# Performance work log

Hardware: AMD Instinct MI355X
Metric: run time of the kernel (lower is better)

The kernel has to match this reference:

```python
import jax, jax.numpy as jnp
import numpy as np

DIM = 256
HEADS = 4
B, N = 2, 4096
NEG = -1e9
EPS = 1e-5


def setup_inputs() -> dict:
    key = jax.random.key(0)
    ks = jax.random.split(key, 12)
    s = 0.02
    inp = {
        "x": jax.random.normal(ks[0], (B, N, DIM), dtype=jnp.float32),
        "adj": jax.random.randint(ks[1], (B, N, N), 0, 2, dtype=jnp.int32),
        "Wq": jax.random.normal(ks[2], (DIM, DIM), dtype=jnp.float32) * s,
        "bq": jnp.zeros((DIM,), jnp.float32),
        "Wk": jax.random.normal(ks[3], (DIM, DIM), dtype=jnp.float32) * s,
        "bk": jnp.zeros((DIM,), jnp.float32),
        "Wv": jax.random.normal(ks[4], (DIM, DIM), dtype=jnp.float32) * s,
        "bv": jnp.zeros((DIM,), jnp.float32),
        "Wo": jax.random.normal(ks[5], (DIM, DIM), dtype=jnp.float32) * s,
        "bo": jnp.zeros((DIM,), jnp.float32),
        "gamma": jnp.ones((DIM,), jnp.float32),
        "beta": jnp.zeros((DIM,), jnp.float32),
    }
    return inp


def reference(x, adj, Wq, bq, Wk, bk, Wv, bv, Wo, bo, gamma, beta):
    Bx, Nx, C = x.shape
    H = HEADS
    D = C // H
    scale = D ** (-0.5)
    # torch Linear: y = x @ W.T + b
    def proj(W, b):
        return (x @ W.T + b).reshape(Bx, Nx, H, D).transpose(0, 2, 1, 3)  # [B,H,N,D]
    q = proj(Wq, bq)
    k = proj(Wk, bk)
    v = proj(Wv, bv)
    attn = jnp.einsum("bhnd,bhmd->bhnm", q, k) * scale          # [B,H,N,N]
    attn = jnp.where(adj[:, None, :, :] == 0, NEG, attn)
    attn = jax.nn.softmax(attn, axis=-1)
    # dropout omitted (eval mode / deterministic reference)
    out = jnp.einsum("bhnm,bhmd->bhnd", attn, v)                # [B,H,N,D]
    out = out.transpose(0, 2, 1, 3).reshape(Bx, Nx, C)
    out = out @ Wo.T + bo
    mu = jnp.mean(out, axis=-1, keepdims=True)
    var = jnp.var(out, axis=-1, keepdims=True)
    return (out - mu) * jax.lax.rsqrt(var + EPS) * gamma + beta
```

## Files before the change

### kernel.cpp

```cpp
#include <hip/hip_runtime.h>
#include <stdint.h>

#define CDIM 256
#define HEADS 4
#define HD 64
#define NB 2
#define NN 4096

typedef unsigned short u16;
typedef unsigned long long u64;
typedef __attribute__((ext_vector_type(8))) short short8;
typedef __attribute__((ext_vector_type(4))) float f32x4;

#define QSCALE 0.1803368801111244f

__device__ __forceinline__ u16 f2bf(float f) {
  union { float f; unsigned u; } v; v.f = f;
  return (u16)((v.u + 0x7fffu + ((v.u >> 16) & 1u)) >> 16);
}
__device__ __forceinline__ float bf2f(u16 u) {
  union { unsigned u; float f; } v; v.u = ((unsigned)u) << 16; return v.f;
}

__global__ __launch_bounds__(256) void prep(
    const int* __restrict__ adj, u64* __restrict__ bm,
    const float* __restrict__ Wq, const float* __restrict__ Wk,
    const float* __restrict__ Wv, const float* __restrict__ Wo,
    u16* __restrict__ Wqb, u16* __restrict__ Wkb,
    u16* __restrict__ Wvb, u16* __restrict__ Wob) {
  if (blockIdx.x < 16384) {
    const int wave = threadIdx.x >> 6, lane = threadIdx.x & 63;
    const size_t widx = (size_t)blockIdx.x * 4 + wave;
    const size_t base = widx * 512;
#pragma unroll
    for (int it = 0; it < 8; ++it) {
      int a = adj[base + it * 64 + lane];
      u64 m = __ballot(a != 0);
      if (lane == 0) bm[widx * 8 + it] = m;
    }
  } else {
    int bi = blockIdx.x - 16384;
    size_t base = ((size_t)bi * 256 + threadIdx.x) * 8;
    int w = (int)(base >> 16);
    size_t lo = base & 65535;
    const float* src;
    u16* dst;
    if (w == 0)      { src = Wq + lo; dst = Wqb + lo; }
    else if (w == 1) { src = Wk + lo; dst = Wkb + lo; }
    else if (w == 2) { src = Wv + lo; dst = Wvb + lo; }
    else             { src = Wo + lo; dst = Wob + lo; }
    float4 a = reinterpret_cast<const float4*>(src)[0];
    float4 b = reinterpret_cast<const float4*>(src)[1];
    short8 h;
    h[0] = (short)f2bf(a.x); h[1] = (short)f2bf(a.y);
    h[2] = (short)f2bf(a.z); h[3] = (short)f2bf(a.w);
    h[4] = (short)f2bf(b.x); h[5] = (short)f2bf(b.y);
    h[6] = (short)f2bf(b.z); h[7] = (short)f2bf(b.w);
    *reinterpret_cast<short8*>(dst) = h;
  }
}

__device__ __forceinline__ short8 fragf32(const float* p) {
  float4 a = reinterpret_cast<const float4*>(p)[0];
  float4 b = reinterpret_cast<const float4*>(p)[1];
  short8 h;
  h[0] = (short)f2bf(a.x); h[1] = (short)f2bf(a.y);
  h[2] = (short)f2bf(a.z); h[3] = (short)f2bf(a.w);
  h[4] = (short)f2bf(b.x); h[5] = (short)f2bf(b.y);
  h[6] = (short)f2bf(b.z); h[7] = (short)f2bf(b.w);
  return h;
}

__global__ __launch_bounds__(256) void qkv_gemm(
    const float* __restrict__ x,
    const u16* __restrict__ Wqb, const u16* __restrict__ Wkb,
    const u16* __restrict__ Wvb,
    const float* __restrict__ bq, const float* __restrict__ bk,
    const float* __restrict__ bv,
    u16* __restrict__ Qb, u16* __restrict__ Kb, u16* __restrict__ Vtb) {
  const int tid = threadIdx.x, w = tid >> 6, lane = tid & 63;
  const int quad = lane >> 4, l15 = lane & 15;
  const int tok0 = blockIdx.x * 16;
  const int b = tok0 >> 12, nl = tok0 & 4095;
  const int ym = blockIdx.y;

  f32x4 acc[4];
#pragma unroll
  for (int i = 0; i < 4; ++i) acc[i] = (f32x4){0.f, 0.f, 0.f, 0.f};

  if (ym < 2) {
    const u16* Wb = (ym == 0) ? Wqb : Wkb;
    const float* bias = (ym == 0) ? bq : bk;
    const float scale = (ym == 0) ? QSCALE : 1.0f;
    u16* outp = (ym == 0) ? Qb : Kb;
#pragma unroll
    for (int ks = 0; ks < 8; ++ks) {
      short8 af = fragf32(x + (size_t)(tok0 + l15) * 256 + ks * 32 + quad * 8);
#pragma unroll
      for (int ns = 0; ns < 4; ++ns) {
        short8 bf = *reinterpret_cast<const short8*>(
            &Wb[(size_t)(w * 64 + ns * 16 + l15) * 256 + ks * 32 + quad * 8]);
        acc[ns] = __builtin_amdgcn_mfma_f32_16x16x32_bf16(af, bf, acc[ns], 0, 0, 0);
      }
    }
#pragma unroll
    for (int ns = 0; ns < 4; ++ns) {
      int d = ns * 16 + l15;
      float bb = bias[w * 64 + d];
#pragma unroll
      for (int r = 0; r < 4; ++r) {
        int tok = nl + quad * 4 + r;
        outp[((size_t)(b * HEADS + w) * NN + tok) * HD + d] =
            f2bf((acc[ns][r] + bb) * scale);
      }
    }
  } else {
#pragma unroll
    for (int ks = 0; ks < 8; ++ks) {
      short8 xf = fragf32(x + (size_t)(tok0 + l15) * 256 + ks * 32 + quad * 8);
#pragma unroll
      for (int ms = 0; ms < 4; ++ms) {
        short8 wf = *reinterpret_cast<const short8*>(
            &Wvb[(size_t)(w * 64 + ms * 16 + l15) * 256 + ks * 32 + quad * 8]);
        acc[ms] = __builtin_amdgcn_mfma_f32_16x16x32_bf16(wf, xf, acc[ms], 0, 0, 0);
      }
    }
#pragma unroll
    for (int ms = 0; ms < 4; ++ms) {
#pragma unroll
      for (int r = 0; r < 4; ++r) {
        int d = ms * 16 + quad * 4 + r;
        float bb = bv[w * 64 + d];
        Vtb[((size_t)((b * HEADS + w) * HD + d)) * NN + nl + l15] =
            f2bf(acc[ms][r] + bb);
      }
    }
  }
}

__global__ __launch_bounds__(256) void attn_mfma(
    const u16* __restrict__ Qb, const u16* __restrict__ Kb,
    const u16* __restrict__ Vtb, const u64* __restrict__ bm,
    u16* __restrict__ Opb, float* __restrict__ Lp) {
  __shared__ u16 Ks[64 * 72];
  __shared__ u16 Vs[64 * 72];
  __shared__ u16 Ps[4][16 * 72];

  const int tid = threadIdx.x;
  const int wave = tid >> 6, lane = tid & 63;
  const int quad = lane >> 4, l15 = lane & 15;
  const int bh = blockIdx.y, b = bh >> 2, h = bh & 3;
  const int q0 = blockIdx.x * 64 + wave * 16;
  const int half = blockIdx.z;
  const int key0 = half * 2048;

  const u16* qr = Qb + ((size_t)bh * NN + q0 + l15) * HD + quad * 8;
  const short8 qf0 = *reinterpret_cast<const short8*>(qr);
  const short8 qf1 = *reinterpret_cast<const short8*>(qr + 32);

  f32x4 Oacc[4];
#pragma unroll
  for (int i = 0; i < 4; ++i) Oacc[i] = (f32x4){0.f, 0.f, 0.f, 0.f};
  float li[4] = {0.f, 0.f, 0.f, 0.f};
  const f32x4 z4 = {0.f, 0.f, 0.f, 0.f};
  u16* Pw = &Ps[wave][0];
  const u64* bmr = bm + ((size_t)b * NN + q0 + quad * 4) * 64 + half * 32;

  const u16* kbase = Kb + (size_t)bh * NN * HD;
  const u16* vbase = Vtb + (size_t)bh * HD * NN;
  const int rr = tid >> 3, cc8 = (tid & 7) * 8;
  const int rr2 = rr + 32;

  uint4 k0, k1, v0, v1;
  k0 = *reinterpret_cast<const uint4*>(kbase + (size_t)(key0 + rr) * HD + cc8);
  k1 = *reinterpret_cast<const uint4*>(kbase + (size_t)(key0 + rr2) * HD + cc8);
  v0 = *reinterpret_cast<const uint4*>(vbase + (size_t)rr * NN + key0 + cc8);
  v1 = *reinterpret_cast<const uint4*>(vbase + (size_t)rr2 * NN + key0 + cc8);

  for (int mt = 0; mt < 32; ++mt) {
    __syncthreads();
    *reinterpret_cast<uint4*>(&Ks[rr * 72 + cc8]) = k0;
    *reinterpret_cast<uint4*>(&Ks[rr2 * 72 + cc8]) = k1;
    *reinterpret_cast<uint4*>(&Vs[rr * 72 + cc8]) = v0;
    *reinterpret_cast<uint4*>(&Vs[rr2 * 72 + cc8]) = v1;
    __syncthreads();
    if (mt + 1 < 32) {
      int kb2 = key0 + (mt + 1) * 64;
      k0 = *reinterpret_cast<const uint4*>(kbase + (size_t)(kb2 + rr) * HD + cc8);
      k1 = *reinterpret_cast<const uint4*>(kbase + (size_t)(kb2 + rr2) * HD + cc8);
      v0 = *reinterpret_cast<const uint4*>(vbase + (size_t)rr * NN + kb2 + cc8);
      v1 = *reinterpret_cast<const uint4*>(vbase + (size_t)rr2 * NN + kb2 + cc8);
    }

    u64 am[4];
#pragma unroll
    for (int r = 0; r < 4; ++r) am[r] = bmr[r * 64 + mt];

#pragma unroll
    for (int t = 0; t < 4; ++t) {
      const u16* kr = &Ks[(t * 16 + l15) * 72 + quad * 8];
      short8 kf0 = *reinterpret_cast<const short8*>(kr);
      short8 kf1 = *reinterpret_cast<const short8*>(kr + 32);
      f32x4 s = __builtin_amdgcn_mfma_f32_16x16x32_bf16(qf0, kf0, z4, 0, 0, 0);
      s = __builtin_amdgcn_mfma_f32_16x16x32_bf16(qf1, kf1, s, 0, 0, 0);
      const int sh = t * 16 + l15;
#pragma unroll
      for (int r = 0; r < 4; ++r) {
        float p = ((unsigned)(am[r] >> sh) & 1u) ? exp2f(s[r]) : 0.f;
        li[r] += p;
        Pw[(quad * 4 + r) * 72 + sh] = (u16)(__float_as_uint(p) >> 16);
      }
    }
    __asm__ volatile("s_waitcnt lgkmcnt(0)" ::: "memory");

    const short8 pf0 = *reinterpret_cast<const short8*>(&Pw[l15 * 72 + quad * 8]);
    const short8 pf1 = *reinterpret_cast<const short8*>(&Pw[l15 * 72 + 32 + quad * 8]);
#pragma unroll
    for (int dt = 0; dt < 4; ++dt) {
      const u16* vr = &Vs[(dt * 16 + l15) * 72 + quad * 8];
      short8 vf0 = *reinterpret_cast<const short8*>(vr);
      short8 vf1 = *reinterpret_cast<const short8*>(vr + 32);
      Oacc[dt] = __builtin_amdgcn_mfma_f32_16x16x32_bf16(pf0, vf0, Oacc[dt], 0, 0, 0);
      Oacc[dt] = __builtin_amdgcn_mfma_f32_16x16x32_bf16(pf1, vf1, Oacc[dt], 0, 0, 0);
    }
  }

  u16* ob = Opb + (size_t)(half * NB + b) * NN * CDIM;
#pragma unroll
  for (int r = 0; r < 4; ++r) {
    float lt = li[r];
#pragma unroll
    for (int off = 1; off < 16; off <<= 1) lt += __shfl_xor(lt, off, 64);
    int tok = q0 + quad * 4 + r;
    if (l15 == 0) Lp[((size_t)half * 8 + bh) * NN + tok] = lt;
#pragma unroll
    for (int dt = 0; dt < 4; ++dt)
      ob[(size_t)tok * CDIM + h * HD + dt * 16 + l15] = f2bf(Oacc[dt][r]);
  }
}

__global__ __launch_bounds__(256) void comb_oproj(
    const u16* __restrict__ Opb, const float* __restrict__ Lp,
    const u16* __restrict__ Wob, const float* __restrict__ bo,
    const float* __restrict__ gamma, const float* __restrict__ beta,
    float* __restrict__ out) {
  __shared__ u16 As[16 * 264];
  __shared__ float ys[16][264];
  __shared__ float linv[64];
  const int tid = threadIdx.x, w = tid >> 6, lane = tid & 63;
  const int quad = lane >> 4, l15 = lane & 15;
  const int tok0 = blockIdx.x * 16;
  const int b = tok0 >> 12, nl = tok0 & 4095;

  if (tid < 64) {
    int tokr = tid >> 2, hh = tid & 3;
    int bh = b * 4 + hh;
    int n = nl + tokr;
    float s = Lp[(size_t)bh * NN + n] + Lp[(size_t)(8 + bh) * NN + n];
    linv[tokr * 4 + hh] = (s > 0.f) ? (1.f / s) : 0.f;
  }
  __syncthreads();

  {
    int tokr = tid >> 4, ch0 = (tid & 15) * 16;
    size_t base = ((size_t)b * NN + nl + tokr) * CDIM + ch0;
    uint4 a0 = *reinterpret_cast<const uint4*>(Opb + base);
    uint4 a1 = *reinterpret_cast<const uint4*>(Opb + base + 8);
    uint4 c0 = *reinterpret_cast<const uint4*>(Opb + 2097152 + base);
    uint4 c1 = *reinterpret_cast<const uint4*>(Opb + 2097152 + base + 8);
    float inv = linv[tokr * 4 + (ch0 >> 6)];
    unsigned wa[8] = {a0.x, a0.y, a0.z, a0.w, a1.x, a1.y, a1.z, a1.w};
    unsigned wb[8] = {c0.x, c0.y, c0.z, c0.w, c1.x, c1.y, c1.z, c1.w};
    u16 ov[16];
#pragma unroll
    for (int i = 0; i < 8; ++i) {
      float lo = (bf2f((u16)(wa[i] & 0xffffu)) + bf2f((u16)(wb[i] & 0xffffu))) * inv;
      float hi = (bf2f((u16)(wa[i] >> 16)) + bf2f((u16)(wb[i] >> 16))) * inv;
      ov[2 * i] = f2bf(lo);
      ov[2 * i + 1] = f2bf(hi);
    }
    u16* dst = &As[tokr * 264 + ch0];
    *reinterpret_cast<uint4*>(dst) = *reinterpret_cast<uint4*>(ov);
    *reinterpret_cast<uint4*>(dst + 8) = *reinterpret_cast<uint4*>(ov + 8);
  }
  __syncthreads();

  f32x4 acc[4];
#pragma unroll
  for (int i = 0; i < 4; ++i) acc[i] = (f32x4){0.f, 0.f, 0.f, 0.f};
#pragma unroll
  for (int ks = 0; ks < 8; ++ks) {
    short8 af = *reinterpret_cast<const short8*>(&As[l15 * 264 + ks * 32 + quad * 8]);
#pragma unroll
    for (int ns = 0; ns < 4; ++ns) {
      short8 bf = *reinterpret_cast<const short8*>(
          &Wob[(size_t)(w * 64 + ns * 16 + l15) * 256 + ks * 32 + quad * 8]);
      acc[ns] = __builtin_amdgcn_mfma_f32_16x16x32_bf16(af, bf, acc[ns], 0, 0, 0);
    }
  }

#pragma unroll
  for (int ns = 0; ns < 4; ++ns) {
    int ch = w * 64 + ns * 16 + l15;
    float bb = bo[ch];
#pragma unroll
    for (int r = 0; r < 4; ++r) ys[quad * 4 + r][ch] = acc[ns][r] + bb;
  }
  __syncthreads();

  float g[4], bt[4];
#pragma unroll
  for (int i = 0; i < 4; ++i) {
    g[i] = gamma[lane + i * 64];
    bt[i] = beta[lane + i * 64];
  }
#pragma unroll
  for (int rr = 0; rr < 4; ++rr) {
    int r = w * 4 + rr;
    float v[4], s = 0.f, s2 = 0.f;
#pragma unroll
    for (int i = 0; i < 4; ++i) {
      v[i] = ys[r][lane + i * 64];
      s += v[i];
      s2 = fmaf(v[i], v[i], s2);
    }
#pragma unroll
    for (int off = 32; off > 0; off >>= 1) {
      s += __shfl_xor(s, off, 64);
      s2 += __shfl_xor(s2, off, 64);
    }
    float mu = s * (1.f / 256.f);
    float rs = rsqrtf(s2 * (1.f / 256.f) - mu * mu + 1e-5f);
    float* orow = out + (size_t)(tok0 + r) * 256;
#pragma unroll
    for (int i = 0; i < 4; ++i)
      orow[lane + i * 64] = (v[i] - mu) * rs * g[i] + bt[i];
  }
}

extern "C" void kernel_launch(void* const* d_in, const int* in_sizes, int n_in,
                              void* d_out, int out_size, void* d_ws, size_t ws_size,
                              hipStream_t stream) {
  const float* x     = (const float*)d_in[0];
  const int*   adj   = (const int*)d_in[1];
  const float* Wq    = (const float*)d_in[2];
  const float* bq    = (const float*)d_in[3];
  const float* Wk    = (const float*)d_in[4];
  const float* bk    = (const float*)d_in[5];
  const float* Wv    = (const float*)d_in[6];
  const float* bv    = (const float*)d_in[7];
  const float* Wo    = (const float*)d_in[8];
  const float* bo    = (const float*)d_in[9];
  const float* gamma = (const float*)d_in[10];
  const float* beta  = (const float*)d_in[11];
  float* out = (float*)d_out;

  const size_t PER = (size_t)NB * HEADS * NN * HD;
  u16* Wqb = (u16*)d_ws;
  u16* Wkb = Wqb + 65536;
  u16* Wvb = Wkb + 65536;
  u16* Wob = Wvb + 65536;
  u64* bmp = (u64*)(Wob + 65536);
  u16* Qb  = (u16*)(bmp + 524288);
  u16* Kb  = Qb + PER;
  u16* Vtb = Kb + PER;
  u16* Opb = Vtb + PER;
  float* Lp = (float*)(Opb + 2 * PER);

  const size_t NEED = (size_t)((u16*)(Lp + 65536) - (u16*)d_ws) * sizeof(u16);
  if (ws_size < NEED) return;

  prep<<<dim3(16512), dim3(256), 0, stream>>>(
      adj, bmp, Wq, Wk, Wv, Wo, Wqb, Wkb, Wvb, Wob);

  qkv_gemm<<<dim3(512, 3), dim3(256), 0, stream>>>(
      x, Wqb, Wkb, Wvb, bq, bk, bv, Qb, Kb, Vtb);

  attn_mfma<<<dim3(NN / 64, NB * HEADS, 2), dim3(256), 0, stream>>>(
      Qb, Kb, Vtb, bmp, Opb, Lp);

  comb_oproj<<<dim3((NB * NN) / 16), dim3(256), 0, stream>>>(
      Opb, Lp, Wob, bo, gamma, beta, out);
}
```

Before: 353.1 us.

## Fuse all stages into one persistent cooperative kernel with grid syncs

```diff
diff --git a/kernel.cpp b/kernel.cpp
--- a/kernel.cpp
+++ b/kernel.cpp
@@ -1,5 +1,8 @@
 #include <hip/hip_runtime.h>
+#include <hip/hip_cooperative_groups.h>
 #include <stdint.h>
+
+namespace cg = cooperative_groups;
 
 #define CDIM 256
 #define HEADS 4
@@ -21,45 +24,6 @@
 __device__ __forceinline__ float bf2f(u16 u) {
   union { unsigned u; float f; } v; v.u = ((unsigned)u) << 16; return v.f;
 }
-
-__global__ __launch_bounds__(256) void prep(
-    const int* __restrict__ adj, u64* __restrict__ bm,
-    const float* __restrict__ Wq, const float* __restrict__ Wk,
-    const float* __restrict__ Wv, const float* __restrict__ Wo,
-    u16* __restrict__ Wqb, u16* __restrict__ Wkb,
-    u16* __restrict__ Wvb, u16* __restrict__ Wob) {
-  if (blockIdx.x < 16384) {
-    const int wave = threadIdx.x >> 6, lane = threadIdx.x & 63;
-    const size_t widx = (size_t)blockIdx.x * 4 + wave;
-    const size_t base = widx * 512;
-#pragma unroll
-    for (int it = 0; it < 8; ++it) {
-      int a = adj[base + it * 64 + lane];
-      u64 m = __ballot(a != 0);
-      if (lane == 0) bm[widx * 8 + it] = m;
-    }
-  } else {
-    int bi = blockIdx.x - 16384;
-    size_t base = ((size_t)bi * 256 + threadIdx.x) * 8;
-    int w = (int)(base >> 16);
-    size_t lo = base & 65535;
-    const float* src;
-    u16* dst;
-    if (w == 0)      { src = Wq + lo; dst = Wqb + lo; }
-    else if (w == 1) { src = Wk + lo; dst = Wkb + lo; }
-    else if (w == 2) { src = Wv + lo; dst = Wvb + lo; }
-    else             { src = Wo + lo; dst = Wob + lo; }
-    float4 a = reinterpret_cast<const float4*>(src)[0];
-    float4 b = reinterpret_cast<const float4*>(src)[1];
-    short8 h;
-    h[0] = (short)f2bf(a.x); h[1] = (short)f2bf(a.y);
-    h[2] = (short)f2bf(a.z); h[3] = (short)f2bf(a.w);
-    h[4] = (short)f2bf(b.x); h[5] = (short)f2bf(b.y);
-    h[6] = (short)f2bf(b.z); h[7] = (short)f2bf(b.w);
-    *reinterpret_cast<short8*>(dst) = h;
-  }
-}
-
 __device__ __forceinline__ short8 fragf32(const float* p) {
   float4 a = reinterpret_cast<const float4*>(p)[0];
   float4 b = reinterpret_cast<const float4*>(p)[1];
@@ -71,8 +35,38 @@
   return h;
 }
 
-__global__ __launch_bounds__(256) void qkv_gemm(
-    const float* __restrict__ x,
+__device__ __forceinline__ void adj_unit(int u, const int* __restrict__ adj,
+                                         u64* __restrict__ bm) {
+  const int wave = threadIdx.x >> 6, lane = threadIdx.x & 63;
+  const size_t widx = (size_t)u * 4 + wave;
+  const size_t base = widx * 512;
+#pragma unroll
+  for (int it = 0; it < 8; ++it) {
+    int a = adj[base + it * 64 + lane];
+    u64 m = __ballot(a != 0);
+    if (lane == 0) bm[widx * 8 + it] = m;
+  }
+}
+
+__device__ __forceinline__ void wconv_unit(
+    int bi, const float* __restrict__ Wq, const float* __restrict__ Wk,
+    const float* __restrict__ Wv, const float* __restrict__ Wo,
+    u16* __restrict__ Wqb, u16* __restrict__ Wkb,
+    u16* __restrict__ Wvb, u16* __restrict__ Wob) {
+  size_t base = ((size_t)bi * 256 + threadIdx.x) * 8;
+  int w = (int)(base >> 16);
+  size_t lo = base & 65535;
+  const float* src;
+  u16* dst;
+  if (w == 0)      { src = Wq + lo; dst = Wqb + lo; }
+  else if (w == 1) { src = Wk + lo; dst = Wkb + lo; }
+  else if (w == 2) { src = Wv + lo; dst = Wvb + lo; }
+  else             { src = Wo + lo; dst = Wob + lo; }
+  *reinterpret_cast<short8*>(dst) = fragf32(src);
+}
+
+__device__ __forceinline__ void qkv_unit(
+    int ym, int bx, const float* __restrict__ x,
     const u16* __restrict__ Wqb, const u16* __restrict__ Wkb,
     const u16* __restrict__ Wvb,
     const float* __restrict__ bq, const float* __restrict__ bk,
@@ -80,9 +74,8 @@
     u16* __restrict__ Qb, u16* __restrict__ Kb, u16* __restrict__ Vtb) {
   const int tid = threadIdx.x, w = tid >> 6, lane = tid & 63;
   const int quad = lane >> 4, l15 = lane & 15;
-  const int tok0 = blockIdx.x * 16;
+  const int tok0 = bx * 16;
   const int b = tok0 >> 12, nl = tok0 & 4095;
-  const int ym = blockIdx.y;
 
   f32x4 acc[4];
 #pragma unroll
@@ -138,20 +131,20 @@
   }
 }
 
-__global__ __launch_bounds__(256) void attn_mfma(
+__device__ __forceinline__ void attn_unit(
+    int bx, int bh, int half, char* smem,
     const u16* __restrict__ Qb, const u16* __restrict__ Kb,
     const u16* __restrict__ Vtb, const u64* __restrict__ bm,
     u16* __restrict__ Opb, float* __restrict__ Lp) {
-  __shared__ u16 Ks[64 * 72];
-  __shared__ u16 Vs[64 * 72];
-  __shared__ u16 Ps[4][16 * 72];
+  u16* Ks = (u16*)smem;
+  u16* Vs = Ks + 64 * 72;
+  u16* Ps = Vs + 64 * 72;
 
   const int tid = threadIdx.x;
   const int wave = tid >> 6, lane = tid & 63;
   const int quad = lane >> 4, l15 = lane & 15;
-  const int bh = blockIdx.y, b = bh >> 2, h = bh & 3;
-  const int q0 = blockIdx.x * 64 + wave * 16;
-  const int half = blockIdx.z;
+  const int b = bh >> 2, h = bh & 3;
+  const int q0 = bx * 64 + wave * 16;
   const int key0 = half * 2048;
 
   const u16* qr = Qb + ((size_t)bh * NN + q0 + l15) * HD + quad * 8;
@@ -163,7 +156,7 @@
   for (int i = 0; i < 4; ++i) Oacc[i] = (f32x4){0.f, 0.f, 0.f, 0.f};
   float li[4] = {0.f, 0.f, 0.f, 0.f};
   const f32x4 z4 = {0.f, 0.f, 0.f, 0.f};
-  u16* Pw = &Ps[wave][0];
+  u16* Pw = Ps + wave * 16 * 72;
   const u64* bmr = bm + ((size_t)b * NN + q0 + quad * 4) * 64 + half * 32;
 
   const u16* kbase = Kb + (size_t)bh * NN * HD;
@@ -225,7 +218,7 @@
     }
   }
 
-  u16* ob = Opb + (size_t)(half * NB + b) * NN * CDIM;
+  u16* ob = Opb + (size_t)(half * NB + (bh >> 2)) * NN * CDIM;
 #pragma unroll
   for (int r = 0; r < 4; ++r) {
     float lt = li[r];
@@ -239,17 +232,17 @@
   }
 }
 
-__global__ __launch_bounds__(256) void comb_oproj(
-    const u16* __restrict__ Opb, const float* __restrict__ Lp,
-    const u16* __restrict__ Wob, const float* __restrict__ bo,
-    const float* __restrict__ gamma, const float* __restrict__ beta,
-    float* __restrict__ out) {
-  __shared__ u16 As[16 * 264];
-  __shared__ float ys[16][264];
-  __shared__ float linv[64];
+__device__ __forceinline__ void comb_unit(
+    int bx, char* smem, const u16* __restrict__ Opb,
+    const float* __restrict__ Lp, const u16* __restrict__ Wob,
+    const float* __restrict__ bo, const float* __restrict__ gamma,
+    const float* __restrict__ beta, float* __restrict__ out) {
+  u16* As = (u16*)smem;
+  float* ys = (float*)(smem + 8448);
+  float* linv = (float*)(smem + 8448 + 16896);
   const int tid = threadIdx.x, w = tid >> 6, lane = tid & 63;
   const int quad = lane >> 4, l15 = lane & 15;
-  const int tok0 = blockIdx.x * 16;
+  const int tok0 = bx * 16;
   const int b = tok0 >> 12, nl = tok0 & 4095;
 
   if (tid < 64) {
@@ -304,7 +297,7 @@
     int ch = w * 64 + ns * 16 + l15;
     float bb = bo[ch];
 #pragma unroll
-    for (int r = 0; r < 4; ++r) ys[quad * 4 + r][ch] = acc[ns][r] + bb;
+    for (int r = 0; r < 4; ++r) ys[(quad * 4 + r) * 264 + ch] = acc[ns][r] + bb;
   }
   __syncthreads();
 
@@ -320,7 +313,7 @@
     float v[4], s = 0.f, s2 = 0.f;
 #pragma unroll
     for (int i = 0; i < 4; ++i) {
-      v[i] = ys[r][lane + i * 64];
+      v[i] = ys[r * 264 + lane + i * 64];
       s += v[i];
       s2 = fmaf(v[i], v[i], s2);
     }
@@ -336,6 +329,62 @@
     for (int i = 0; i < 4; ++i)
       orow[lane + i * 64] = (v[i] - mu) * rs * g[i] + bt[i];
   }
+}
+
+__global__ __launch_bounds__(256, 4) void fused(
+    const float* x, const int* adj,
+    const float* Wq, const float* bq, const float* Wk, const float* bk,
+    const float* Wv, const float* bv, const float* Wo, const float* bo,
+    const float* gamma, const float* beta, float* out,
+    u16* Wqb, u16* Wkb, u16* Wvb, u16* Wob, u64* bmp,
+    u16* Qb, u16* Kb, u16* Vtb, u16* Opb, float* Lp) {
+  __shared__ __align__(16) char smem[27648];
+  const int blk = blockIdx.x;
+  cg::grid_group grid = cg::this_grid();
+
+  if (blk < 128) wconv_unit(blk, Wq, Wk, Wv, Wo, Wqb, Wkb, Wvb, Wob);
+#pragma unroll 1
+  for (int i = 0; i < 8; ++i) adj_unit(blk * 8 + i, adj, bmp);
+  grid.sync();
+
+#pragma unroll 1
+  for (int u = blk; u < 1536; u += 1024)
+    qkv_unit(u >> 9, u & 511, x, Wqb, Wkb, Wvb, bq, bk, bv, Qb, Kb, Vtb);
+#pragma unroll 1
+  for (int i = 0; i < 8; ++i) adj_unit(8192 + blk * 8 + i, adj, bmp);
+  grid.sync();
+
+  attn_unit(blk & 63, (blk >> 6) & 7, blk >> 9, smem,
+            Qb, Kb, Vtb, bmp, Opb, Lp);
+  grid.sync();
+
+  if (blk < 512)
+    comb_unit(blk, smem, Opb, Lp, Wob, bo, gamma, beta, out);
+}
+
+__global__ __launch_bounds__(256) void prep_k(
+    const int* adj, u64* bmp, const float* Wq, const float* Wk,
+    const float* Wv, const float* Wo, u16* Wqb, u16* Wkb, u16* Wvb, u16* Wob) {
+  if (blockIdx.x < 16384) adj_unit(blockIdx.x, adj, bmp);
+  else wconv_unit(blockIdx.x - 16384, Wq, Wk, Wv, Wo, Wqb, Wkb, Wvb, Wob);
+}
+__global__ __launch_bounds__(256) void qkv_k(
+    const float* x, const u16* Wqb, const u16* Wkb, const u16* Wvb,
+    const float* bq, const float* bk, const float* bv,
+    u16* Qb, u16* Kb, u16* Vtb) {
+  qkv_unit(blockIdx.y, blockIdx.x, x, Wqb, Wkb, Wvb, bq, bk, bv, Qb, Kb, Vtb);
+}
+__global__ __launch_bounds__(256) void attn_k(
+    const u16* Qb, const u16* Kb, const u16* Vtb, const u64* bmp,
+    u16* Opb, float* Lp) {
+  __shared__ __align__(16) char smem[27648];
+  attn_unit(blockIdx.x, blockIdx.y, blockIdx.z, smem, Qb, Kb, Vtb, bmp, Opb, Lp);
+}
+__global__ __launch_bounds__(256) void comb_k(
+    const u16* Opb, const float* Lp, const u16* Wob, const float* bo,
+    const float* gamma, const float* beta, float* out) {
+  __shared__ __align__(16) char smem[25600];
+  comb_unit(blockIdx.x, smem, Opb, Lp, Wob, bo, gamma, beta, out);
 }
 
 extern "C" void kernel_launch(void* const* d_in, const int* in_sizes, int n_in,
@@ -370,15 +419,24 @@
   const size_t NEED = (size_t)((u16*)(Lp + 65536) - (u16*)d_ws) * sizeof(u16);
   if (ws_size < NEED) return;
 
-  prep<<<dim3(16512), dim3(256), 0, stream>>>(
-      adj, bmp, Wq, Wk, Wv, Wo, Wqb, Wkb, Wvb, Wob);
-
-  qkv_gemm<<<dim3(512, 3), dim3(256), 0, stream>>>(
-      x, Wqb, Wkb, Wvb, bq, bk, bv, Qb, Kb, Vtb);
-
-  attn_mfma<<<dim3(NN / 64, NB * HEADS, 2), dim3(256), 0, stream>>>(
-      Qb, Kb, Vtb, bmp, Opb, Lp);
-
-  comb_oproj<<<dim3((NB * NN) / 16), dim3(256), 0, stream>>>(
-      Opb, Lp, Wob, bo, gamma, beta, out);
-}
+  void* args[] = {
+      (void*)&x, (void*)&adj, (void*)&Wq, (void*)&bq, (void*)&Wk, (void*)&bk,
+      (void*)&Wv, (void*)&bv, (void*)&Wo, (void*)&bo, (void*)&gamma,
+      (void*)&beta, (void*)&out, (void*)&Wqb, (void*)&Wkb, (void*)&Wvb,
+      (void*)&Wob, (void*)&bmp, (void*)&Qb, (void*)&Kb, (void*)&Vtb,
+      (void*)&Opb, (void*)&Lp};
+  hipError_t rc = hipLaunchCooperativeKernel(
+      (void*)fused, dim3(1024), dim3(256), args, 0, stream);
+
+  if (rc != hipSuccess) {
+    (void)hipGetLastError();
+    prep_k<<<dim3(16512), dim3(256), 0, stream>>>(
+        adj, bmp, Wq, Wk, Wv, Wo, Wqb, Wkb, Wvb, Wob);
+    qkv_k<<<dim3(512, 3), dim3(256), 0, stream>>>(
+        x, Wqb, Wkb, Wvb, bq, bk, bv, Qb, Kb, Vtb);
+    attn_k<<<dim3(64, 8, 2), dim3(256), 0, stream>>>(
+        Qb, Kb, Vtb, bmp, Opb, Lp);
+    comb_k<<<dim3(512), dim3(256), 0, stream>>>(
+        Opb, Lp, Wob, bo, gamma, beta, out);
+  }
+}
```

Result: slower. 764.6 us (+116.5%).

## Merge prep and QKV GEMM into one launch; compute row sums via MFMA

Applied to the files above, without the earlier changes.

```diff
diff --git a/kernel.cpp b/kernel.cpp
--- a/kernel.cpp
+++ b/kernel.cpp
@@ -21,45 +21,6 @@
 __device__ __forceinline__ float bf2f(u16 u) {
   union { unsigned u; float f; } v; v.u = ((unsigned)u) << 16; return v.f;
 }
-
-__global__ __launch_bounds__(256) void prep(
-    const int* __restrict__ adj, u64* __restrict__ bm,
-    const float* __restrict__ Wq, const float* __restrict__ Wk,
-    const float* __restrict__ Wv, const float* __restrict__ Wo,
-    u16* __restrict__ Wqb, u16* __restrict__ Wkb,
-    u16* __restrict__ Wvb, u16* __restrict__ Wob) {
-  if (blockIdx.x < 16384) {
-    const int wave = threadIdx.x >> 6, lane = threadIdx.x & 63;
-    const size_t widx = (size_t)blockIdx.x * 4 + wave;
-    const size_t base = widx * 512;
-#pragma unroll
-    for (int it = 0; it < 8; ++it) {
-      int a = adj[base + it * 64 + lane];
-      u64 m = __ballot(a != 0);
-      if (lane == 0) bm[widx * 8 + it] = m;
-    }
-  } else {
-    int bi = blockIdx.x - 16384;
-    size_t base = ((size_t)bi * 256 + threadIdx.x) * 8;
-    int w = (int)(base >> 16);
-    size_t lo = base & 65535;
-    const float* src;
-    u16* dst;
-    if (w == 0)      { src = Wq + lo; dst = Wqb + lo; }
-    else if (w == 1) { src = Wk + lo; dst = Wkb + lo; }
-    else if (w == 2) { src = Wv + lo; dst = Wvb + lo; }
-    else             { src = Wo + lo; dst = Wob + lo; }
-    float4 a = reinterpret_cast<const float4*>(src)[0];
-    float4 b = reinterpret_cast<const float4*>(src)[1];
-    short8 h;
-    h[0] = (short)f2bf(a.x); h[1] = (short)f2bf(a.y);
-    h[2] = (short)f2bf(a.z); h[3] = (short)f2bf(a.w);
-    h[4] = (short)f2bf(b.x); h[5] = (short)f2bf(b.y);
-    h[6] = (short)f2bf(b.z); h[7] = (short)f2bf(b.w);
-    *reinterpret_cast<short8*>(dst) = h;
-  }
-}
-
 __device__ __forceinline__ short8 fragf32(const float* p) {
   float4 a = reinterpret_cast<const float4*>(p)[0];
   float4 b = reinterpret_cast<const float4*>(p)[1];
@@ -71,25 +32,37 @@
   return h;
 }
 
-__global__ __launch_bounds__(256) void qkv_gemm(
-    const float* __restrict__ x,
-    const u16* __restrict__ Wqb, const u16* __restrict__ Wkb,
-    const u16* __restrict__ Wvb,
+__device__ __forceinline__ void adj_unit(int u, const int* __restrict__ adj,
+                                         u64* __restrict__ bm) {
+  const int wave = threadIdx.x >> 6, lane = threadIdx.x & 63;
+  const size_t widx = (size_t)u * 4 + wave;
+  const size_t base = widx * 512;
+#pragma unroll
+  for (int it = 0; it < 8; ++it) {
+    int a = adj[base + it * 64 + lane];
+    u64 m = __ballot(a != 0);
+    if (lane == 0) bm[widx * 8 + it] = m;
+  }
+}
+
+__device__ __forceinline__ void qkv_unit(
+    int ym, int bx, const float* __restrict__ x,
+    const float* __restrict__ Wq, const float* __restrict__ Wk,
+    const float* __restrict__ Wv,
     const float* __restrict__ bq, const float* __restrict__ bk,
     const float* __restrict__ bv,
     u16* __restrict__ Qb, u16* __restrict__ Kb, u16* __restrict__ Vtb) {
   const int tid = threadIdx.x, w = tid >> 6, lane = tid & 63;
   const int quad = lane >> 4, l15 = lane & 15;
-  const int tok0 = blockIdx.x * 16;
+  const int tok0 = bx * 16;
   const int b = tok0 >> 12, nl = tok0 & 4095;
-  const int ym = blockIdx.y;
 
   f32x4 acc[4];
 #pragma unroll
   for (int i = 0; i < 4; ++i) acc[i] = (f32x4){0.f, 0.f, 0.f, 0.f};
 
   if (ym < 2) {
-    const u16* Wb = (ym == 0) ? Wqb : Wkb;
+    const float* W = (ym == 0) ? Wq : Wk;
     const float* bias = (ym == 0) ? bq : bk;
     const float scale = (ym == 0) ? QSCALE : 1.0f;
     u16* outp = (ym == 0) ? Qb : Kb;
@@ -98,8 +71,8 @@
       short8 af = fragf32(x + (size_t)(tok0 + l15) * 256 + ks * 32 + quad * 8);
 #pragma unroll
       for (int ns = 0; ns < 4; ++ns) {
-        short8 bf = *reinterpret_cast<const short8*>(
-            &Wb[(size_t)(w * 64 + ns * 16 + l15) * 256 + ks * 32 + quad * 8]);
+        short8 bf = fragf32(
+            W + (size_t)(w * 64 + ns * 16 + l15) * 256 + ks * 32 + quad * 8);
         acc[ns] = __builtin_amdgcn_mfma_f32_16x16x32_bf16(af, bf, acc[ns], 0, 0, 0);
       }
     }
@@ -120,8 +93,8 @@
       short8 xf = fragf32(x + (size_t)(tok0 + l15) * 256 + ks * 32 + quad * 8);
 #pragma unroll
       for (int ms = 0; ms < 4; ++ms) {
-        short8 wf = *reinterpret_cast<const short8*>(
-            &Wvb[(size_t)(w * 64 + ms * 16 + l15) * 256 + ks * 32 + quad * 8]);
+        short8 wf = fragf32(
+            Wv + (size_t)(w * 64 + ms * 16 + l15) * 256 + ks * 32 + quad * 8);
         acc[ms] = __builtin_amdgcn_mfma_f32_16x16x32_bf16(wf, xf, acc[ms], 0, 0, 0);
       }
     }
@@ -135,6 +108,25 @@
             f2bf(acc[ms][r] + bb);
       }
     }
+  }
+}
+
+__global__ __launch_bounds__(256) void l1_prep_qkv(
+    const float* __restrict__ x, const int* __restrict__ adj,
+    const float* __restrict__ Wq, const float* __restrict__ Wk,
+    const float* __restrict__ Wv, const float* __restrict__ Wo,
+    const float* __restrict__ bq, const float* __restrict__ bk,
+    const float* __restrict__ bv,
+    u64* __restrict__ bmp, u16* __restrict__ Qb, u16* __restrict__ Kb,
+    u16* __restrict__ Vtb, u16* __restrict__ Wob) {
+  const int blk = blockIdx.x;
+  if (blk < 1536) {
+    qkv_unit(blk >> 9, blk & 511, x, Wq, Wk, Wv, bq, bk, bv, Qb, Kb, Vtb);
+  } else if (blk < 17920) {
+    adj_unit(blk - 1536, adj, bmp);
+  } else {
+    size_t base = ((size_t)(blk - 17920) * 256 + threadIdx.x) * 8;
+    *reinterpret_cast<short8*>(Wob + base) = fragf32(Wo + base);
   }
 }
 
@@ -158,10 +150,14 @@
   const short8 qf0 = *reinterpret_cast<const short8*>(qr);
   const short8 qf1 = *reinterpret_cast<const short8*>(qr + 32);
 
+  short8 ones;
+#pragma unroll
+  for (int i = 0; i < 8; ++i) ones[i] = (short)0x3F80;
+
   f32x4 Oacc[4];
 #pragma unroll
   for (int i = 0; i < 4; ++i) Oacc[i] = (f32x4){0.f, 0.f, 0.f, 0.f};
-  float li[4] = {0.f, 0.f, 0.f, 0.f};
+  f32x4 Oli = (f32x4){0.f, 0.f, 0.f, 0.f};
   const f32x4 z4 = {0.f, 0.f, 0.f, 0.f};
   u16* Pw = &Ps[wave][0];
   const u64* bmr = bm + ((size_t)b * NN + q0 + quad * 4) * 64 + half * 32;
@@ -204,17 +200,29 @@
       f32x4 s = __builtin_amdgcn_mfma_f32_16x16x32_bf16(qf0, kf0, z4, 0, 0, 0);
       s = __builtin_amdgcn_mfma_f32_16x16x32_bf16(qf1, kf1, s, 0, 0, 0);
       const int sh = t * 16 + l15;
+      float pr[4];
+#pragma unroll
+      for (int r = 0; r < 4; ++r)
+        pr[r] = ((unsigned)(am[r] >> sh) & 1u) ? exp2f(s[r]) : 0.f;
+      unsigned pk[4];
 #pragma unroll
       for (int r = 0; r < 4; ++r) {
-        float p = ((unsigned)(am[r] >> sh) & 1u) ? exp2f(s[r]) : 0.f;
-        li[r] += p;
-        Pw[(quad * 4 + r) * 72 + sh] = (u16)(__float_as_uint(p) >> 16);
+        unsigned pv = __float_as_uint(pr[r]);
+        unsigned nb = __float_as_uint(__shfl_xor(pr[r], 1, 64));
+        pk[r] = (pv >> 16) | (nb & 0xffff0000u);
+      }
+      if ((l15 & 1) == 0) {
+#pragma unroll
+        for (int r = 0; r < 4; ++r)
+          *reinterpret_cast<unsigned*>(&Pw[(quad * 4 + r) * 72 + sh]) = pk[r];
       }
     }
     __asm__ volatile("s_waitcnt lgkmcnt(0)" ::: "memory");
 
     const short8 pf0 = *reinterpret_cast<const short8*>(&Pw[l15 * 72 + quad * 8]);
     const short8 pf1 = *reinterpret_cast<const short8*>(&Pw[l15 * 72 + 32 + quad * 8]);
+    Oli = __builtin_amdgcn_mfma_f32_16x16x32_bf16(pf0, ones, Oli, 0, 0, 0);
+    Oli = __builtin_amdgcn_mfma_f32_16x16x32_bf16(pf1, ones, Oli, 0, 0, 0);
 #pragma unroll
     for (int dt = 0; dt < 4; ++dt) {
       const u16* vr = &Vs[(dt * 16 + l15) * 72 + quad * 8];
@@ -228,11 +236,8 @@
   u16* ob = Opb + (size_t)(half * NB + b) * NN * CDIM;
 #pragma unroll
   for (int r = 0; r < 4; ++r) {
-    float lt = li[r];
-#pragma unroll
-    for (int off = 1; off < 16; off <<= 1) lt += __shfl_xor(lt, off, 64);
     int tok = q0 + quad * 4 + r;
-    if (l15 == 0) Lp[((size_t)half * 8 + bh) * NN + tok] = lt;
+    if (l15 == 0) Lp[((size_t)half * 8 + bh) * NN + tok] = Oli[r];
 #pragma unroll
     for (int dt = 0; dt < 4; ++dt)
       ob[(size_t)tok * CDIM + h * HD + dt * 16 + l15] = f2bf(Oacc[dt][r]);
@@ -356,10 +361,7 @@
   float* out = (float*)d_out;
 
   const size_t PER = (size_t)NB * HEADS * NN * HD;
-  u16* Wqb = (u16*)d_ws;
-  u16* Wkb = Wqb + 65536;
-  u16* Wvb = Wkb + 65536;
-  u16* Wob = Wvb + 65536;
+  u16* Wob = (u16*)d_ws;
   u64* bmp = (u64*)(Wob + 65536);
   u16* Qb  = (u16*)(bmp + 524288);
   u16* Kb  = Qb + PER;
@@ -370,11 +372,8 @@
   const size_t NEED = (size_t)((u16*)(Lp + 65536) - (u16*)d_ws) * sizeof(u16);
   if (ws_size < NEED) return;
 
-  prep<<<dim3(16512), dim3(256), 0, stream>>>(
-      adj, bmp, Wq, Wk, Wv, Wo, Wqb, Wkb, Wvb, Wob);
-
-  qkv_gemm<<<dim3(512, 3), dim3(256), 0, stream>>>(
-      x, Wqb, Wkb, Wvb, bq, bk, bv, Qb, Kb, Vtb);
+  l1_prep_qkv<<<dim3(17952), dim3(256), 0, stream>>>(
+      x, adj, Wq, Wk, Wv, Wo, bq, bk, bv, bmp, Qb, Kb, Vtb, Wob);
 
   attn_mfma<<<dim3(NN / 64, NB * HEADS, 2), dim3(256), 0, stream>>>(
       Qb, Kb, Vtb, bmp, Opb, Lp);
```

Result: slower. 381.2 us (+8.0%).

## Vectorize adjacency bitmask packing, pair P stores, compute row sums via MFMA

Applied to the files above, without the earlier changes.

```diff
diff --git a/kernel.cpp b/kernel.cpp
--- a/kernel.cpp
+++ b/kernel.cpp
@@ -8,6 +8,7 @@
 #define NN 4096
 
 typedef unsigned short u16;
+typedef unsigned char u8;
 typedef unsigned long long u64;
 typedef __attribute__((ext_vector_type(8))) short short8;
 typedef __attribute__((ext_vector_type(4))) float f32x4;
@@ -21,45 +22,6 @@
 __device__ __forceinline__ float bf2f(u16 u) {
   union { unsigned u; float f; } v; v.u = ((unsigned)u) << 16; return v.f;
 }
-
-__global__ __launch_bounds__(256) void prep(
-    const int* __restrict__ adj, u64* __restrict__ bm,
-    const float* __restrict__ Wq, const float* __restrict__ Wk,
-    const float* __restrict__ Wv, const float* __restrict__ Wo,
-    u16* __restrict__ Wqb, u16* __restrict__ Wkb,
-    u16* __restrict__ Wvb, u16* __restrict__ Wob) {
-  if (blockIdx.x < 16384) {
-    const int wave = threadIdx.x >> 6, lane = threadIdx.x & 63;
-    const size_t widx = (size_t)blockIdx.x * 4 + wave;
-    const size_t base = widx * 512;
-#pragma unroll
-    for (int it = 0; it < 8; ++it) {
-      int a = adj[base + it * 64 + lane];
-      u64 m = __ballot(a != 0);
-      if (lane == 0) bm[widx * 8 + it] = m;
-    }
-  } else {
-    int bi = blockIdx.x - 16384;
-    size_t base = ((size_t)bi * 256 + threadIdx.x) * 8;
-    int w = (int)(base >> 16);
-    size_t lo = base & 65535;
-    const float* src;
-    u16* dst;
-    if (w == 0)      { src = Wq + lo; dst = Wqb + lo; }
-    else if (w == 1) { src = Wk + lo; dst = Wkb + lo; }
-    else if (w == 2) { src = Wv + lo; dst = Wvb + lo; }
-    else             { src = Wo + lo; dst = Wob + lo; }
-    float4 a = reinterpret_cast<const float4*>(src)[0];
-    float4 b = reinterpret_cast<const float4*>(src)[1];
-    short8 h;
-    h[0] = (short)f2bf(a.x); h[1] = (short)f2bf(a.y);
-    h[2] = (short)f2bf(a.z); h[3] = (short)f2bf(a.w);
-    h[4] = (short)f2bf(b.x); h[5] = (short)f2bf(b.y);
-    h[6] = (short)f2bf(b.z); h[7] = (short)f2bf(b.w);
-    *reinterpret_cast<short8*>(dst) = h;
-  }
-}
-
 __device__ __forceinline__ short8 fragf32(const float* p) {
   float4 a = reinterpret_cast<const float4*>(p)[0];
   float4 b = reinterpret_cast<const float4*>(p)[1];
@@ -69,6 +31,48 @@
   h[4] = (short)f2bf(b.x); h[5] = (short)f2bf(b.y);
   h[6] = (short)f2bf(b.z); h[7] = (short)f2bf(b.w);
   return h;
+}
+
+__global__ __launch_bounds__(256) void prep(
+    const int* __restrict__ adj, u8* __restrict__ bmb,
+    const float* __restrict__ Wq, const float* __restrict__ Wk,
+    const float* __restrict__ Wv, const float* __restrict__ Wo,
+    u16* __restrict__ Wqb, u16* __restrict__ Wkb,
+    u16* __restrict__ Wvb, u16* __restrict__ Wob) {
+  const int blk = blockIdx.x;
+  if (blk < 4096) {
+    const int wave = threadIdx.x >> 6, lane = threadIdx.x & 63;
+    const int c0 = blk * 16 + wave * 4;
+#pragma unroll
+    for (int it = 0; it < 4; ++it) {
+      int c = c0 + it;
+      int row = c >> 3, kb = (c & 7) * 512;
+      const int* src = adj + (size_t)row * 4096 + kb + lane * 8;
+      uint4 a = *reinterpret_cast<const uint4*>(src);
+      uint4 b = *reinterpret_cast<const uint4*>(src + 4);
+      unsigned byte = 0;
+      byte |= (a.x != 0) ? 1u : 0u;
+      byte |= (a.y != 0) ? 2u : 0u;
+      byte |= (a.z != 0) ? 4u : 0u;
+      byte |= (a.w != 0) ? 8u : 0u;
+      byte |= (b.x != 0) ? 16u : 0u;
+      byte |= (b.y != 0) ? 32u : 0u;
+      byte |= (b.z != 0) ? 64u : 0u;
+      byte |= (b.w != 0) ? 128u : 0u;
+      bmb[(size_t)row * 512 + (c & 7) * 64 + lane] = (u8)byte;
+    }
+  } else {
+    size_t base = ((size_t)(blk - 4096) * 256 + threadIdx.x) * 8;
+    int w = (int)(base >> 16);
+    size_t lo = base & 65535;
+    const float* src;
+    u16* dst;
+    if (w == 0)      { src = Wq + lo; dst = Wqb + lo; }
+    else if (w == 1) { src = Wk + lo; dst = Wkb + lo; }
+    else if (w == 2) { src = Wv + lo; dst = Wvb + lo; }
+    else             { src = Wo + lo; dst = Wob + lo; }
+    *reinterpret_cast<short8*>(dst) = fragf32(src);
+  }
 }
 
 __global__ __launch_bounds__(256) void qkv_gemm(
@@ -158,10 +162,14 @@
   const short8 qf0 = *reinterpret_cast<const short8*>(qr);
   const short8 qf1 = *reinterpret_cast<const short8*>(qr + 32);
 
+  short8 ones;
+#pragma unroll
+  for (int i = 0; i < 8; ++i) ones[i] = (short)0x3F80;
+
   f32x4 Oacc[4];
 #pragma unroll
   for (int i = 0; i < 4; ++i) Oacc[i] = (f32x4){0.f, 0.f, 0.f, 0.f};
-  float li[4] = {0.f, 0.f, 0.f, 0.f};
+  f32x4 Oli = (f32x4){0.f, 0.f, 0.f, 0.f};
   const f32x4 z4 = {0.f, 0.f, 0.f, 0.f};
   u16* Pw = &Ps[wave][0];
   const u64* bmr = bm + ((size_t)b * NN + q0 + quad * 4) * 64 + half * 32;
@@ -204,17 +212,29 @@
       f32x4 s = __builtin_amdgcn_mfma_f32_16x16x32_bf16(qf0, kf0, z4, 0, 0, 0);
       s = __builtin_amdgcn_mfma_f32_16x16x32_bf16(qf1, kf1, s, 0, 0, 0);
       const int sh = t * 16 + l15;
+      float pr[4];
+#pragma unroll
+      for (int r = 0; r < 4; ++r)
+        pr[r] = ((unsigned)(am[r] >> sh) & 1u) ? exp2f(s[r]) : 0.f;
+      unsigned pk[4];
 #pragma unroll
       for (int r = 0; r < 4; ++r) {
-        float p = ((unsigned)(am[r] >> sh) & 1u) ? exp2f(s[r]) : 0.f;
-        li[r] += p;
-        Pw[(quad * 4 + r) * 72 + sh] = (u16)(__float_as_uint(p) >> 16);
+        unsigned pv = __float_as_uint(pr[r]);
+        unsigned nb = __float_as_uint(__shfl_xor(pr[r], 1, 64));
+        pk[r] = (pv >> 16) | (nb & 0xffff0000u);
+      }
+      if ((l15 & 1) == 0) {
+#pragma unroll
+        for (int r = 0; r < 4; ++r)
+          *reinterpret_cast<unsigned*>(&Pw[(quad * 4 + r) * 72 + sh]) = pk[r];
       }
     }
     __asm__ volatile("s_waitcnt lgkmcnt(0)" ::: "memory");
 
     const short8 pf0 = *reinterpret_cast<const short8*>(&Pw[l15 * 72 + quad * 8]);
     const short8 pf1 = *reinterpret_cast<const short8*>(&Pw[l15 * 72 + 32 + quad * 8]);
+    Oli = __builtin_amdgcn_mfma_f32_16x16x32_bf16(pf0, ones, Oli, 0, 0, 0);
+    Oli = __builtin_amdgcn_mfma_f32_16x16x32_bf16(pf1, ones, Oli, 0, 0, 0);
 #pragma unroll
     for (int dt = 0; dt < 4; ++dt) {
       const u16* vr = &Vs[(dt * 16 + l15) * 72 + quad * 8];
@@ -228,11 +248,8 @@
   u16* ob = Opb + (size_t)(half * NB + b) * NN * CDIM;
 #pragma unroll
   for (int r = 0; r < 4; ++r) {
-    float lt = li[r];
-#pragma unroll
-    for (int off = 1; off < 16; off <<= 1) lt += __shfl_xor(lt, off, 64);
     int tok = q0 + quad * 4 + r;
-    if (l15 == 0) Lp[((size_t)half * 8 + bh) * NN + tok] = lt;
+    if (l15 == 0) Lp[((size_t)half * 8 + bh) * NN + tok] = Oli[r];
 #pragma unroll
     for (int dt = 0; dt < 4; ++dt)
       ob[(size_t)tok * CDIM + h * HD + dt * 16 + l15] = f2bf(Oacc[dt][r]);
@@ -370,8 +387,8 @@
   const size_t NEED = (size_t)((u16*)(Lp + 65536) - (u16*)d_ws) * sizeof(u16);
   if (ws_size < NEED) return;
 
-  prep<<<dim3(16512), dim3(256), 0, stream>>>(
-      adj, bmp, Wq, Wk, Wv, Wo, Wqb, Wkb, Wvb, Wob);
+  prep<<<dim3(4224), dim3(256), 0, stream>>>(
+      adj, (u8*)bmp, Wq, Wk, Wv, Wo, Wqb, Wkb, Wvb, Wob);
 
   qkv_gemm<<<dim3(512, 3), dim3(256), 0, stream>>>(
       x, Wqb, Wkb, Wvb, bq, bk, bv, Qb, Kb, Vtb);
```

Result: no change. 350.5 us (-0.7%).
